# Kernel tuning notes

Measured on AMD Instinct MI355X. Metric: run time of the kernel, lower is better.

Reference implementation:

```python
import jax, jax.numpy as jnp
import numpy as np
from jax import lax

INPUT_DIM = 16
H1 = 5
H2 = 50
NUM_CLASSES = 20
B = 4096
T = 512


def _lstm(x, w_ih, w_hh, b_ih, b_hh, hidden):
    # x: [B, T, D]; PyTorch LSTM gate order i, f, g, o; returns all hidden states [B, T, H]
    xg = jnp.einsum('btd,gd->btg', x, w_ih) + (b_ih + b_hh)  # [B, T, 4H]
    xg_t = jnp.swapaxes(xg, 0, 1)  # [T, B, 4H]
    h0 = jnp.zeros((x.shape[0], hidden), x.dtype)
    c0 = jnp.zeros((x.shape[0], hidden), x.dtype)

    def step(carry, xt):
        h, c = carry
        g = xt + h @ w_hh.T  # [B, 4H]
        i, f, gg, o = jnp.split(g, 4, axis=-1)
        i = jax.nn.sigmoid(i)
        f = jax.nn.sigmoid(f)
        gg = jnp.tanh(gg)
        o = jax.nn.sigmoid(o)
        c = f * c + i * gg
        h = o * jnp.tanh(c)
        return (h, c), h

    _, hs = lax.scan(step, (h0, c0), xg_t)
    return jnp.swapaxes(hs, 0, 1)  # [B, T, H]


def setup_inputs() -> dict:
    key = jax.random.key(0)
    ks = jax.random.split(key, 12)
    s1 = 1.0 / np.sqrt(H1)
    s2 = 1.0 / np.sqrt(H2)
    u = lambda k, shape, s: jax.random.uniform(k, shape, jnp.float32, -s, s)
    return {
        'x': jax.random.normal(ks[0], (B, T, INPUT_DIM), jnp.float32),
        'w_ih1': u(ks[1], (4 * H1, INPUT_DIM), s1),
        'w_hh1': u(ks[2], (4 * H1, H1), s1),
        'b_ih1': u(ks[3], (4 * H1,), s1),
        'b_hh1': u(ks[4], (4 * H1,), s1),
        'w_ih2': u(ks[5], (4 * H2, H1), s2),
        'w_hh2': u(ks[6], (4 * H2, H2), s2),
        'b_ih2': u(ks[7], (4 * H2,), s2),
        'b_hh2': u(ks[8], (4 * H2,), s2),
        'fc_w': u(ks[9], (NUM_CLASSES, H2), s2),
        'fc_b': u(ks[10], (NUM_CLASSES,), s2),
    }


def reference(x, w_ih1, w_hh1, b_ih1, b_hh1, w_ih2, w_hh2, b_ih2, b_hh2, fc_w, fc_b):
    h1 = _lstm(x, w_ih1, w_hh1, b_ih1, b_hh1, H1)   # [B, T, 5]
    h2 = _lstm(h1, w_ih2, w_hh2, b_ih2, b_hh2, H2)  # [B, T, 50]
    feat = h2[:, -1, :]  # last timestep; dropout is identity in eval mode
    out = feat @ fc_w.T + fc_b  # [B, num_classes]
    return (out, feat)
```

## Files before the change

### kernel.cpp

```cpp
#include <hip/hip_runtime.h>
#include <stdint.h>

#define B_TOTAL 4096
#define T_STEPS 512
#define IN_DIM 16
#define H1 5
#define H2 50
#define NCLS 20

typedef __attribute__((ext_vector_type(8))) short bf16x8;
typedef __attribute__((ext_vector_type(4))) float f32x4;

#define LOG2E 1.44269504f
__device__ inline float sigm(float x){
  float e = __builtin_amdgcn_exp2f(-LOG2E * x);
  return __builtin_amdgcn_rcpf(1.0f + e);
}
__device__ inline float tanh_(float x){
  float e = __builtin_amdgcn_exp2f((2.0f*LOG2E) * x);
  float r = __builtin_amdgcn_rcpf(1.0f + e);
  return fmaf(-2.0f, r, 1.0f);
}
__device__ inline unsigned pack_top(float a, float b){
  return __builtin_amdgcn_perm(__float_as_uint(a), __float_as_uint(b), 0x07060302u);
}
__device__ inline void cvt_store(unsigned short* dh, unsigned short* dl, float4 v){
  uint2 H, L;
  H.x = pack_top(v.y, v.x);
  H.y = pack_top(v.w, v.z);
  float r0 = v.x - __uint_as_float(__float_as_uint(v.x) & 0xFFFF0000u);
  float r1 = v.y - __uint_as_float(__float_as_uint(v.y) & 0xFFFF0000u);
  float r2 = v.z - __uint_as_float(__float_as_uint(v.z) & 0xFFFF0000u);
  float r3 = v.w - __uint_as_float(__float_as_uint(v.w) & 0xFFFF0000u);
  L.x = pack_top(r1, r0);
  L.y = pack_top(r3, r2);
  *(uint2*)dh = H; *(uint2*)dl = L;
}
__device__ inline void split1(float h, unsigned short& hi, unsigned short& lo){
  unsigned u = __float_as_uint(h);
  hi = (unsigned short)(u >> 16);
  float r = h - __uint_as_float(u & 0xFFFF0000u);
  lo = (unsigned short)(__float_as_uint(r) >> 16);
}
__device__ inline void wsplit(float w, short& hi, short& lo){
  unsigned u = __float_as_uint(w);
  hi = (short)(u >> 16);
  float r = w - __uint_as_float(u & 0xFFFF0000u);
  lo = (short)(__float_as_uint(r) >> 16);
}

#define LDS_FENCE() __asm__ volatile("s_waitcnt lgkmcnt(0)" ::: "memory")
#define BARRIER()   __asm__ volatile("s_barrier" ::: "memory")

__global__ __launch_bounds__(320, 1) void lstm_fused_kernel(
    const float* __restrict__ x,
    const float* __restrict__ w_ih1, const float* __restrict__ w_hh1,
    const float* __restrict__ b_ih1, const float* __restrict__ b_hh1,
    const float* __restrict__ w_ih2, const float* __restrict__ w_hh2,
    const float* __restrict__ b_ih2, const float* __restrict__ b_hh2,
    const float* __restrict__ fc_w, const float* __restrict__ fc_b,
    float* __restrict__ out)
{
  const int tid  = threadIdx.x;
  const int lane = tid & 63;
  const int wave = tid >> 6;
  const int l15  = lane & 15;
  const int quad = lane >> 4;
  const int b0   = blockIdx.x * 16;

  __shared__ __align__(16) unsigned short a2h[2][16*72], a2l[2][16*72];
  __shared__ __align__(16) unsigned short xrh[8][16*24], xrl[8][16*24];
  __shared__ __align__(16) unsigned short a1h[16*24], a1l[16*24];
  __shared__ float h2f[16*52];

  bf16x8 Bh[4][2], Bl[4][2];
  float bias[4];
  float cst[4] = {0.f,0.f,0.f,0.f};
  const int cg = wave*16 + l15;

  if (wave < 4){
    bool valid = cg < H2;
#pragma unroll
    for (int tt=0; tt<4; ++tt){
      int grow = tt*H2 + cg;
#pragma unroll
      for (int kt=0; kt<2; ++kt){
#pragma unroll
        for (int j=0;j<8;j++){
          int kk = kt*32 + quad*8 + j;
          float w = 0.f;
          if (valid){
            if (kk < H2)         w = w_hh2[grow*H2 + kk];
            else if (kk < H2+H1) w = w_ih2[grow*H1 + (kk-H2)];
          }
          short hi, lo; wsplit(w, hi, lo);
          Bh[tt][kt][j] = hi; Bl[tt][kt][j] = lo;
        }
      }
      bias[tt] = valid ? (b_ih2[grow] + b_hh2[grow]) : 0.f;
    }
  } else {
    bool valid = l15 < H1;
#pragma unroll
    for (int tt=0; tt<4; ++tt){
      int grow = tt*H1 + l15;
#pragma unroll
      for (int j=0;j<8;j++){
        int kk = quad*8 + j;
        float w = 0.f;
        if (valid){
          if (kk < IN_DIM)         w = w_ih1[grow*IN_DIM + kk];
          else if (kk < IN_DIM+H1) w = w_hh1[grow*H1 + (kk-IN_DIM)];
        }
        short hi, lo; wsplit(w, hi, lo);
        Bh[tt][0][j] = hi; Bl[tt][0][j] = lo;
        Bh[tt][1][j] = 0;  Bl[tt][1][j] = 0;
      }
      bias[tt] = valid ? (b_ih1[grow] + b_hh1[grow]) : 0.f;
    }
  }

  { unsigned short* p = &a2h[0][0]; for (int i=tid;i<2*16*72;i+=320) p[i]=0; }
  { unsigned short* p = &a2l[0][0]; for (int i=tid;i<2*16*72;i+=320) p[i]=0; }
  { unsigned short* p = &a1h[0];    for (int i=tid;i<16*24;i+=320)   p[i]=0; }
  { unsigned short* p = &a1l[0];    for (int i=tid;i<16*24;i+=320)   p[i]=0; }

  const int xb = lane >> 2;
  const int xd = (lane & 3) * 4;
  if (wave == 4){
#pragma unroll
    for (int s=0;s<8;s++){
      float4 v = *(const float4*)&x[((size_t)(b0+xb)*T_STEPS + s)*IN_DIM + xd];
      cvt_store(&xrh[s][xb*24+xd], &xrl[s][xb*24+xd], v);
    }
  }
  __syncthreads();

  float4 pf0, pf1, pf2, pf3;
  bool pend = false;

  for (int t=-1; t<T_STEPS; ++t){
    const int rd = t & 1;
    const int wr = rd ^ 1;

    if (wave == 4){
      const int s = t + 1;
      if (s < T_STEPS){
        if ((s & 3) == 0 && s+4 < T_STEPS){
          const float* xp = &x[((size_t)(b0+xb)*T_STEPS + (s+4))*IN_DIM + xd];
          pf0 = *(const float4*)(xp + 0*IN_DIM);
          pf1 = *(const float4*)(xp + 1*IN_DIM);
          pf2 = *(const float4*)(xp + 2*IN_DIM);
          pf3 = *(const float4*)(xp + 3*IN_DIM);
          pend = true;
        }
        const int slot = s & 7;
        bf16x8 ah, al;
        if (quad < 2){
          ah = *(const bf16x8*)&xrh[slot][l15*24 + quad*8];
          al = *(const bf16x8*)&xrl[slot][l15*24 + quad*8];
        } else {
          ah = *(const bf16x8*)&a1h[l15*24 + (quad-2)*8];
          al = *(const bf16x8*)&a1l[l15*24 + (quad-2)*8];
        }
        f32x4 acc[4];
#pragma unroll
        for (int tt=0; tt<4; ++tt){
          f32x4 cA = {bias[tt],bias[tt],bias[tt],bias[tt]};
          cA = __builtin_amdgcn_mfma_f32_16x16x32_bf16(ah, Bh[tt][0], cA, 0,0,0);
          f32x4 cB = {0.f,0.f,0.f,0.f};
          cB = __builtin_amdgcn_mfma_f32_16x16x32_bf16(al, Bh[tt][0], cB, 0,0,0);
          cB = __builtin_amdgcn_mfma_f32_16x16x32_bf16(ah, Bl[tt][0], cB, 0,0,0);
          acc[tt] = cA + cB;
        }
#pragma unroll
        for (int r=0;r<4;r++){
          float gi = sigm(acc[0][r]);
          float gf = sigm(acc[1][r]);
          float gg = tanh_(acc[2][r]);
          float go = sigm(acc[3][r]);
          cst[r] = gf*cst[r] + gi*gg;
          float h = go * tanh_(cst[r]);
          if (l15 < H1){
            unsigned short hh, hl; split1(h, hh, hl);
            int row = quad*4 + r;
            a1h[row*24 + l15] = hh;
            a1l[row*24 + l15] = hl;
            a2h[wr][row*72 + H2 + l15] = hh;
            a2l[wr][row*72 + H2 + l15] = hl;
          }
        }
        if ((s & 3) == 2 && pend){
          cvt_store(&xrh[(s+2)&7][xb*24+xd], &xrl[(s+2)&7][xb*24+xd], pf0);
          cvt_store(&xrh[(s+3)&7][xb*24+xd], &xrl[(s+3)&7][xb*24+xd], pf1);
          cvt_store(&xrh[(s+4)&7][xb*24+xd], &xrl[(s+4)&7][xb*24+xd], pf2);
          cvt_store(&xrh[(s+5)&7][xb*24+xd], &xrl[(s+5)&7][xb*24+xd], pf3);
          pend = false;
        }
      }
    } else if (t >= 0){
      const int rb = l15*72;
      bf16x8 ah0 = *(const bf16x8*)&a2h[rd][rb +      quad*8];
      bf16x8 al0 = *(const bf16x8*)&a2l[rd][rb +      quad*8];
      bf16x8 ah1 = *(const bf16x8*)&a2h[rd][rb + 32 + quad*8];
      bf16x8 al1 = *(const bf16x8*)&a2l[rd][rb + 32 + quad*8];

      f32x4 acc[4];
#pragma unroll
      for (int tt=0; tt<4; ++tt){
        f32x4 c0 = {bias[tt],bias[tt],bias[tt],bias[tt]};
        c0 = __builtin_amdgcn_mfma_f32_16x16x32_bf16(ah0, Bh[tt][0], c0, 0,0,0);
        c0 = __builtin_amdgcn_mfma_f32_16x16x32_bf16(al0, Bh[tt][0], c0, 0,0,0);
        f32x4 c1 = {0.f,0.f,0.f,0.f};
        c1 = __builtin_amdgcn_mfma_f32_16x16x32_bf16(ah0, Bl[tt][0], c1, 0,0,0);
        c1 = __builtin_amdgcn_mfma_f32_16x16x32_bf16(ah1, Bh[tt][1], c1, 0,0,0);
        f32x4 c2 = {0.f,0.f,0.f,0.f};
        c2 = __builtin_amdgcn_mfma_f32_16x16x32_bf16(al1, Bh[tt][1], c2, 0,0,0);
        c2 = __builtin_amdgcn_mfma_f32_16x16x32_bf16(ah1, Bl[tt][1], c2, 0,0,0);
        acc[tt] = (c0 + c1) + c2;
      }
      const bool act = cg < H2;
#pragma unroll
      for (int r=0;r<4;r++){
        float gi = sigm(acc[0][r]);
        float gf = sigm(acc[1][r]);
        float gg = tanh_(acc[2][r]);
        float go = sigm(acc[3][r]);
        cst[r] = gf*cst[r] + gi*gg;
        float h = go * tanh_(cst[r]);
        if (act){
          unsigned short hh, hl; split1(h, hh, hl);
          int row = quad*4 + r;
          a2h[wr][row*72 + cg] = hh;
          a2l[wr][row*72 + cg] = hl;
          if (t == T_STEPS-1){
            out[(size_t)B_TOTAL*NCLS + (size_t)(b0+row)*H2 + cg] = h;
            h2f[row*52 + cg] = h;
          }
        }
      }
    }

    LDS_FENCE();
    BARRIER();
  }

  __syncthreads();
  {
    int b = tid / 20, o = tid % 20;
    float s = fc_b[o];
#pragma unroll 10
    for (int k=0;k<H2;k++) s += fc_w[o*H2+k] * h2f[b*52+k];
    out[(size_t)(b0+b)*NCLS + o] = s;
  }
}

extern "C" void kernel_launch(void* const* d_in, const int* in_sizes, int n_in,
                              void* d_out, int out_size, void* d_ws, size_t ws_size,
                              hipStream_t stream) {
  const float* x     = (const float*)d_in[0];
  const float* w_ih1 = (const float*)d_in[1];
  const float* w_hh1 = (const float*)d_in[2];
  const float* b_ih1 = (const float*)d_in[3];
  const float* b_hh1 = (const float*)d_in[4];
  const float* w_ih2 = (const float*)d_in[5];
  const float* w_hh2 = (const float*)d_in[6];
  const float* b_ih2 = (const float*)d_in[7];
  const float* b_hh2 = (const float*)d_in[8];
  const float* fc_w  = (const float*)d_in[9];
  const float* fc_b  = (const float*)d_in[10];
  float* out = (float*)d_out;

  lstm_fused_kernel<<<dim3(B_TOTAL/16), dim3(320), 0, stream>>>(
      x, w_ih1, w_hh1, b_ih1, b_hh1, w_ih2, w_hh2, b_ih2, b_hh2, fc_w, fc_b, out);
}
```

Measured before the change: 723.5 us.

## Fold activation log2 scaling into weights and unroll timestep loop by two

Pre-scales the gate weights and biases by log2e (2·log2e for the tanh gate) so the sigmoid and tanh exp2 arguments need no per-step multiply. The time loop is unrolled by two so the double-buffer indices become compile-time constants. MFMA accumulation is restructured into two chains seeded directly from a precomputed bias vector. Together these cut per-step VALU and address work on the serial recurrence critical path, at the cost of slightly different rounding from splitting the scaled weights into bf16.

```diff
diff --git a/kernel.cpp b/kernel.cpp
--- a/kernel.cpp
+++ b/kernel.cpp
@@ -12,15 +12,12 @@
 typedef __attribute__((ext_vector_type(4))) float f32x4;
 
 #define LOG2E 1.44269504f
-__device__ inline float sigm(float x){
-  float e = __builtin_amdgcn_exp2f(-LOG2E * x);
-  return __builtin_amdgcn_rcpf(1.0f + e);
-}
-__device__ inline float tanh_(float x){
-  float e = __builtin_amdgcn_exp2f((2.0f*LOG2E) * x);
-  float r = __builtin_amdgcn_rcpf(1.0f + e);
-  return fmaf(-2.0f, r, 1.0f);
-}
+#define C2L   2.88539008f
+
+__device__ inline float rcp1pexp2(float y){
+  return __builtin_amdgcn_rcpf(1.0f + __builtin_amdgcn_exp2f(y));
+}
+
 __device__ inline unsigned pack_top(float a, float b){
   return __builtin_amdgcn_perm(__float_as_uint(a), __float_as_uint(b), 0x07060302u);
 }
@@ -82,6 +79,7 @@
     bool valid = cg < H2;
 #pragma unroll
     for (int tt=0; tt<4; ++tt){
+      const float gsc = (tt == 2) ? C2L : LOG2E;
       int grow = tt*H2 + cg;
 #pragma unroll
       for (int kt=0; kt<2; ++kt){
@@ -93,16 +91,18 @@
             if (kk < H2)         w = w_hh2[grow*H2 + kk];
             else if (kk < H2+H1) w = w_ih2[grow*H1 + (kk-H2)];
           }
+          w *= gsc;
           short hi, lo; wsplit(w, hi, lo);
           Bh[tt][kt][j] = hi; Bl[tt][kt][j] = lo;
         }
       }
-      bias[tt] = valid ? (b_ih2[grow] + b_hh2[grow]) : 0.f;
+      bias[tt] = valid ? gsc * (b_ih2[grow] + b_hh2[grow]) : 0.f;
     }
   } else {
     bool valid = l15 < H1;
 #pragma unroll
     for (int tt=0; tt<4; ++tt){
+      const float gsc = (tt == 2) ? C2L : LOG2E;
       int grow = tt*H1 + l15;
 #pragma unroll
       for (int j=0;j<8;j++){
@@ -112,13 +112,22 @@
           if (kk < IN_DIM)         w = w_ih1[grow*IN_DIM + kk];
           else if (kk < IN_DIM+H1) w = w_hh1[grow*H1 + (kk-IN_DIM)];
         }
+        w *= gsc;
         short hi, lo; wsplit(w, hi, lo);
         Bh[tt][0][j] = hi; Bl[tt][0][j] = lo;
         Bh[tt][1][j] = 0;  Bl[tt][1][j] = 0;
       }
-      bias[tt] = valid ? (b_ih1[grow] + b_hh1[grow]) : 0.f;
-    }
-  }
+      bias[tt] = valid ? gsc * (b_ih1[grow] + b_hh1[grow]) : 0.f;
+    }
+  }
+
+  f32x4 biasv[4];
+#pragma unroll
+  for (int tt=0; tt<4; ++tt){
+    biasv[tt][0] = bias[tt]; biasv[tt][1] = bias[tt];
+    biasv[tt][2] = bias[tt]; biasv[tt][3] = bias[tt];
+  }
+  const f32x4 zero4 = {0.f,0.f,0.f,0.f};
 
   { unsigned short* p = &a2h[0][0]; for (int i=tid;i<2*16*72;i+=320) p[i]=0; }
   { unsigned short* p = &a2l[0][0]; for (int i=tid;i<2*16*72;i+=320) p[i]=0; }
@@ -139,111 +148,120 @@
   float4 pf0, pf1, pf2, pf3;
   bool pend = false;
 
-  for (int t=-1; t<T_STEPS; ++t){
-    const int rd = t & 1;
-    const int wr = rd ^ 1;
-
-    if (wave == 4){
-      const int s = t + 1;
-      if (s < T_STEPS){
-        if ((s & 3) == 0 && s+4 < T_STEPS){
-          const float* xp = &x[((size_t)(b0+xb)*T_STEPS + (s+4))*IN_DIM + xd];
-          pf0 = *(const float4*)(xp + 0*IN_DIM);
-          pf1 = *(const float4*)(xp + 1*IN_DIM);
-          pf2 = *(const float4*)(xp + 2*IN_DIM);
-          pf3 = *(const float4*)(xp + 3*IN_DIM);
-          pend = true;
-        }
-        const int slot = s & 7;
-        bf16x8 ah, al;
-        if (quad < 2){
-          ah = *(const bf16x8*)&xrh[slot][l15*24 + quad*8];
-          al = *(const bf16x8*)&xrl[slot][l15*24 + quad*8];
-        } else {
-          ah = *(const bf16x8*)&a1h[l15*24 + (quad-2)*8];
-          al = *(const bf16x8*)&a1l[l15*24 + (quad-2)*8];
-        }
-        f32x4 acc[4];
-#pragma unroll
-        for (int tt=0; tt<4; ++tt){
-          f32x4 cA = {bias[tt],bias[tt],bias[tt],bias[tt]};
-          cA = __builtin_amdgcn_mfma_f32_16x16x32_bf16(ah, Bh[tt][0], cA, 0,0,0);
-          f32x4 cB = {0.f,0.f,0.f,0.f};
-          cB = __builtin_amdgcn_mfma_f32_16x16x32_bf16(al, Bh[tt][0], cB, 0,0,0);
-          cB = __builtin_amdgcn_mfma_f32_16x16x32_bf16(ah, Bl[tt][0], cB, 0,0,0);
-          acc[tt] = cA + cB;
-        }
-#pragma unroll
-        for (int r=0;r<4;r++){
-          float gi = sigm(acc[0][r]);
-          float gf = sigm(acc[1][r]);
-          float gg = tanh_(acc[2][r]);
-          float go = sigm(acc[3][r]);
-          cst[r] = gf*cst[r] + gi*gg;
-          float h = go * tanh_(cst[r]);
-          if (l15 < H1){
-            unsigned short hh, hl; split1(h, hh, hl);
-            int row = quad*4 + r;
-            a1h[row*24 + l15] = hh;
-            a1l[row*24 + l15] = hl;
-            a2h[wr][row*72 + H2 + l15] = hh;
-            a2l[wr][row*72 + H2 + l15] = hl;
-          }
-        }
-        if ((s & 3) == 2 && pend){
-          cvt_store(&xrh[(s+2)&7][xb*24+xd], &xrl[(s+2)&7][xb*24+xd], pf0);
-          cvt_store(&xrh[(s+3)&7][xb*24+xd], &xrl[(s+3)&7][xb*24+xd], pf1);
-          cvt_store(&xrh[(s+4)&7][xb*24+xd], &xrl[(s+4)&7][xb*24+xd], pf2);
-          cvt_store(&xrh[(s+5)&7][xb*24+xd], &xrl[(s+5)&7][xb*24+xd], pf3);
-          pend = false;
-        }
-      }
-    } else if (t >= 0){
-      const int rb = l15*72;
-      bf16x8 ah0 = *(const bf16x8*)&a2h[rd][rb +      quad*8];
-      bf16x8 al0 = *(const bf16x8*)&a2l[rd][rb +      quad*8];
-      bf16x8 ah1 = *(const bf16x8*)&a2h[rd][rb + 32 + quad*8];
-      bf16x8 al1 = *(const bf16x8*)&a2l[rd][rb + 32 + quad*8];
-
-      f32x4 acc[4];
-#pragma unroll
-      for (int tt=0; tt<4; ++tt){
-        f32x4 c0 = {bias[tt],bias[tt],bias[tt],bias[tt]};
-        c0 = __builtin_amdgcn_mfma_f32_16x16x32_bf16(ah0, Bh[tt][0], c0, 0,0,0);
-        c0 = __builtin_amdgcn_mfma_f32_16x16x32_bf16(al0, Bh[tt][0], c0, 0,0,0);
-        f32x4 c1 = {0.f,0.f,0.f,0.f};
-        c1 = __builtin_amdgcn_mfma_f32_16x16x32_bf16(ah0, Bl[tt][0], c1, 0,0,0);
-        c1 = __builtin_amdgcn_mfma_f32_16x16x32_bf16(ah1, Bh[tt][1], c1, 0,0,0);
-        f32x4 c2 = {0.f,0.f,0.f,0.f};
-        c2 = __builtin_amdgcn_mfma_f32_16x16x32_bf16(al1, Bh[tt][1], c2, 0,0,0);
-        c2 = __builtin_amdgcn_mfma_f32_16x16x32_bf16(ah1, Bl[tt][1], c2, 0,0,0);
-        acc[tt] = (c0 + c1) + c2;
-      }
-      const bool act = cg < H2;
-#pragma unroll
-      for (int r=0;r<4;r++){
-        float gi = sigm(acc[0][r]);
-        float gf = sigm(acc[1][r]);
-        float gg = tanh_(acc[2][r]);
-        float go = sigm(acc[3][r]);
-        cst[r] = gf*cst[r] + gi*gg;
-        float h = go * tanh_(cst[r]);
-        if (act){
-          unsigned short hh, hl; split1(h, hh, hl);
-          int row = quad*4 + r;
-          a2h[wr][row*72 + cg] = hh;
-          a2l[wr][row*72 + cg] = hl;
-          if (t == T_STEPS-1){
-            out[(size_t)B_TOTAL*NCLS + (size_t)(b0+row)*H2 + cg] = h;
-            h2f[row*52 + cg] = h;
-          }
-        }
-      }
-    }
-
-    LDS_FENCE();
-    BARRIER();
-  }
+#define ACT_BLOCK(ACC_, HV_) \
+    _Pragma("unroll") \
+    for (int r=0;r<4;r++){ \
+      float gi = rcp1pexp2(-ACC_[0][r]); \
+      float gf = rcp1pexp2(-ACC_[1][r]); \
+      float gg = fmaf(-2.0f, rcp1pexp2(ACC_[2][r]), 1.0f); \
+      float go = rcp1pexp2(-ACC_[3][r]); \
+      cst[r] = fmaf(gf, cst[r], gi * (C2L * gg)); \
+      HV_[r] = go * fmaf(-2.0f, rcp1pexp2(cst[r]), 1.0f); \
+    }
+
+#define LSTM2_BODY(T_, RD_, WR_) do { \
+    const int rb = l15*72; \
+    bf16x8 ah0 = *(const bf16x8*)&a2h[RD_][rb +      quad*8]; \
+    bf16x8 al0 = *(const bf16x8*)&a2l[RD_][rb +      quad*8]; \
+    bf16x8 ah1 = *(const bf16x8*)&a2h[RD_][rb + 32 + quad*8]; \
+    bf16x8 al1 = *(const bf16x8*)&a2l[RD_][rb + 32 + quad*8]; \
+    f32x4 acc[4]; \
+    _Pragma("unroll") \
+    for (int tt=0; tt<4; ++tt){ \
+      f32x4 c0 = __builtin_amdgcn_mfma_f32_16x16x32_bf16(ah0, Bh[tt][0], biasv[tt], 0,0,0); \
+      c0 = __builtin_amdgcn_mfma_f32_16x16x32_bf16(al0, Bh[tt][0], c0, 0,0,0); \
+      c0 = __builtin_amdgcn_mfma_f32_16x16x32_bf16(ah0, Bl[tt][0], c0, 0,0,0); \
+      f32x4 c1 = __builtin_amdgcn_mfma_f32_16x16x32_bf16(ah1, Bh[tt][1], zero4, 0,0,0); \
+      c1 = __builtin_amdgcn_mfma_f32_16x16x32_bf16(al1, Bh[tt][1], c1, 0,0,0); \
+      c1 = __builtin_amdgcn_mfma_f32_16x16x32_bf16(ah1, Bl[tt][1], c1, 0,0,0); \
+      acc[tt] = c0 + c1; \
+    } \
+    float hv[4]; \
+    ACT_BLOCK(acc, hv) \
+    if (cg < H2){ \
+      const int wrb = quad*4*72 + cg; \
+      _Pragma("unroll") \
+      for (int r=0;r<4;r++){ \
+        unsigned short hh, hl; split1(hv[r], hh, hl); \
+        a2h[WR_][wrb + r*72] = hh; \
+        a2l[WR_][wrb + r*72] = hl; \
+      } \
+      if ((T_) == T_STEPS-1){ \
+        _Pragma("unroll") \
+        for (int r=0;r<4;r++){ \
+          out[(size_t)B_TOTAL*NCLS + (size_t)(b0+quad*4+r)*H2 + cg] = hv[r]; \
+          h2f[(quad*4+r)*52 + cg] = hv[r]; \
+        } \
+      } \
+    } \
+  } while(0)
+
+#define LSTM1_BODY(T_, WR_) do { \
+    const int s = (T_) + 1; \
+    if (s < T_STEPS){ \
+      if ((s & 3) == 0 && s+4 < T_STEPS){ \
+        const float* xp = &x[((size_t)(b0+xb)*T_STEPS + (s+4))*IN_DIM + xd]; \
+        pf0 = *(const float4*)(xp + 0*IN_DIM); \
+        pf1 = *(const float4*)(xp + 1*IN_DIM); \
+        pf2 = *(const float4*)(xp + 2*IN_DIM); \
+        pf3 = *(const float4*)(xp + 3*IN_DIM); \
+        pend = true; \
+      } \
+      const int slot = s & 7; \
+      bf16x8 ah, al; \
+      if (quad < 2){ \
+        ah = *(const bf16x8*)&xrh[slot][l15*24 + quad*8]; \
+        al = *(const bf16x8*)&xrl[slot][l15*24 + quad*8]; \
+      } else { \
+        ah = *(const bf16x8*)&a1h[l15*24 + (quad-2)*8]; \
+        al = *(const bf16x8*)&a1l[l15*24 + (quad-2)*8]; \
+      } \
+      f32x4 acc[4]; \
+      _Pragma("unroll") \
+      for (int tt=0; tt<4; ++tt){ \
+        f32x4 c0 = __builtin_amdgcn_mfma_f32_16x16x32_bf16(ah, Bh[tt][0], biasv[tt], 0,0,0); \
+        c0 = __builtin_amdgcn_mfma_f32_16x16x32_bf16(al, Bh[tt][0], c0, 0,0,0); \
+        c0 = __builtin_amdgcn_mfma_f32_16x16x32_bf16(ah, Bl[tt][0], c0, 0,0,0); \
+        acc[tt] = c0; \
+      } \
+      float hv[4]; \
+      ACT_BLOCK(acc, hv) \
+      if (l15 < H1){ \
+        _Pragma("unroll") \
+        for (int r=0;r<4;r++){ \
+          unsigned short hh, hl; split1(hv[r], hh, hl); \
+          const int row = quad*4 + r; \
+          a1h[row*24 + l15] = hh; \
+          a1l[row*24 + l15] = hl; \
+          a2h[WR_][row*72 + H2 + l15] = hh; \
+          a2l[WR_][row*72 + H2 + l15] = hl; \
+        } \
+      } \
+      if ((s & 3) == 2 && pend){ \
+        cvt_store(&xrh[(s+2)&7][xb*24+xd], &xrl[(s+2)&7][xb*24+xd], pf0); \
+        cvt_store(&xrh[(s+3)&7][xb*24+xd], &xrl[(s+3)&7][xb*24+xd], pf1); \
+        cvt_store(&xrh[(s+4)&7][xb*24+xd], &xrl[(s+4)&7][xb*24+xd], pf2); \
+        cvt_store(&xrh[(s+5)&7][xb*24+xd], &xrl[(s+5)&7][xb*24+xd], pf3); \
+        pend = false; \
+      } \
+    } \
+  } while(0)
+
+  if (wave == 4) LSTM1_BODY(-1, 0);
+  LDS_FENCE(); BARRIER();
+
+  for (int t2 = 0; t2 < T_STEPS; t2 += 2){
+    if (wave == 4) LSTM1_BODY(t2, 1);
+    else           LSTM2_BODY(t2, 0, 1);
+    LDS_FENCE(); BARRIER();
+    if (wave == 4) LSTM1_BODY(t2+1, 0);
+    else           LSTM2_BODY(t2+1, 1, 0);
+    LDS_FENCE(); BARRIER();
+  }
+
+#undef LSTM2_BODY
+#undef LSTM1_BODY
+#undef ACT_BLOCK
 
   __syncthreads();
   {
```

Measured after the change: 633.8 us. -12.4%, faster.
